# Kernel tuning notes

Measured on AMD Instinct MI355X. Metric: run time of the kernel, lower is better.

The kernel has to match this reference:

```python
import jax, jax.numpy as jnp
import numpy as np

N = 100000
IN_C = 128
HID = 128
LAT = 64
E = 800000


def gcn_conv(x, src, dst, norm, W, b, num_nodes):
    # x: [N, Cin]; src/dst: [E+N] (self-loops appended); norm: [E+N]
    xw = x @ W                                   # [N, Cout]
    msg = xw[src] * norm[:, None]                # gather + scale, [E+N, Cout]
    out = jax.ops.segment_sum(msg, dst, num_segments=num_nodes)
    return out + b


def setup_inputs() -> dict:
    key = jax.random.key(0)
    ks = jax.random.split(key, 8)
    x = jax.random.normal(ks[0], (N, IN_C), dtype=jnp.float32)
    edge_index = jax.random.randint(ks[1], (2, E), 0, N, dtype=jnp.int64)
    batch = jnp.zeros((N,), dtype=jnp.int64)
    # GCNConv params (Glorot-ish scale)
    W1 = jax.random.normal(ks[2], (IN_C, HID), dtype=jnp.float32) / np.sqrt(IN_C)
    b1 = jnp.zeros((HID,), dtype=jnp.float32)
    Wmu = jax.random.normal(ks[3], (HID, LAT), dtype=jnp.float32) / np.sqrt(HID)
    bmu = jnp.zeros((LAT,), dtype=jnp.float32)
    Wlv = jax.random.normal(ks[4], (HID, LAT), dtype=jnp.float32) / np.sqrt(HID)
    blv = jnp.zeros((LAT,), dtype=jnp.float32)
    return {"x": x, "edge_index": edge_index, "batch": batch,
            "W1": W1, "b1": b1, "Wmu": Wmu, "bmu": bmu, "Wlv": Wlv, "blv": blv}


def reference(x, edge_index, batch, W1, b1, Wmu, bmu, Wlv, blv):
    num_nodes = x.shape[0]
    loop = jnp.arange(num_nodes, dtype=edge_index.dtype)
    src = jnp.concatenate([edge_index[0], loop])   # source nodes (+self loops)
    dst = jnp.concatenate([edge_index[1], loop])   # target nodes (+self loops)
    # symmetric GCN normalization: deg over targets, norm = d[src]^-1/2 * d[dst]^-1/2
    deg = jax.ops.segment_sum(jnp.ones_like(dst, dtype=x.dtype), dst,
                              num_segments=num_nodes)
    dis = jnp.where(deg > 0, jax.lax.rsqrt(deg), 0.0)
    norm = dis[src] * dis[dst]                      # [E+N]

    h = jax.nn.relu(gcn_conv(x, src, dst, norm, W1, b1, num_nodes))
    mu = gcn_conv(h, src, dst, norm, Wmu, bmu, num_nodes)
    logvar = gcn_conv(h, src, dst, norm, Wlv, blv, num_nodes)
    return (mu, logvar)
```

## Files before the change

kernel.cpp:

```cpp
#include <hip/hip_runtime.h>

typedef short bf16x8 __attribute__((ext_vector_type(8)));
typedef float f32x4 __attribute__((ext_vector_type(4)));

#define ELLK 32
#define OCAP 4096

static __device__ __forceinline__ float4 f4zero() { return make_float4(0.f, 0.f, 0.f, 0.f); }

static __device__ __forceinline__ unsigned short f2bf(float f) {
  unsigned u = __float_as_uint(f);
  u += 0x7FFFu + ((u >> 16) & 1u);
  return (unsigned short)(u >> 16);
}
static __device__ __forceinline__ float2 bf2x2(unsigned u) {
  float2 r;
  r.x = __uint_as_float(u << 16);
  r.y = __uint_as_float(u & 0xFFFF0000u);
  return r;
}

__global__ void k_setup(const float* __restrict__ W1, const float* __restrict__ Wmu,
                        const float* __restrict__ Wlv, unsigned short* __restrict__ Wt1,
                        unsigned short* __restrict__ Wt2, int* __restrict__ cnt,
                        int* __restrict__ ocount, int n, int nbz) {
  int b = blockIdx.x;
  if (b < nbz) {
    int i = b * 256 + threadIdx.x;
    if (i < n) cnt[i] = 0;
    if (b == 0 && threadIdx.x == 0) *ocount = 0;
  } else {
    int id = (b - nbz) * 256 + threadIdx.x;
    if (id < 16384) {
      int nn = id >> 7, k = id & 127;
      Wt1[id] = f2bf(W1[k * 128 + nn]);
    } else {
      int id2 = id - 16384;
      int nn = id2 >> 7, k = id2 & 127;
      float v = (nn < 64) ? Wmu[k * 64 + nn] : Wlv[k * 64 + (nn - 64)];
      Wt2[id2] = f2bf(v);
    }
  }
}

__global__ __launch_bounds__(256) void k_gemm1_fill(
    const float* __restrict__ x, const unsigned short* __restrict__ Wt,
    unsigned short* __restrict__ A, const int* __restrict__ ei,
    int* __restrict__ cnt, int* __restrict__ ell, int2* __restrict__ ovf,
    int* __restrict__ ocount, int n, int E, int gblk) {
  __shared__ unsigned short Wl[128 * 136];
  __shared__ unsigned short Xl[64 * 136];
  if (blockIdx.x >= gblk) {
    int e = (blockIdx.x - gblk) * 256 + threadIdx.x;
    if (e < E) {
      int s = ei[e];
      int d = ei[E + e];
      int pos = atomicAdd(&cnt[d], 1);
      if (pos < ELLK) {
        ell[d * ELLK + pos] = s;
      } else {
        int o = atomicAdd(ocount, 1);
        if (o < OCAP) ovf[o] = make_int2(d, s);
      }
    }
    return;
  }
  const int tid = threadIdx.x;
  const int row0 = blockIdx.x * 64;
  {
    const uint4* Wg = (const uint4*)Wt;
#pragma unroll
    for (int i = 0; i < 8; ++i) {
      int idx = tid + i * 256;
      int r = idx >> 4, c = idx & 15;
      *(uint4*)&Wl[r * 136 + c * 8] = Wg[r * 16 + c];
    }
  }
  {
#pragma unroll
    for (int i = 0; i < 8; ++i) {
      int idx = tid + i * 256;
      int r = idx >> 5, c = idx & 31;
      int gi = row0 + r;
      float4 v = (gi < n) ? ((const float4*)x)[(size_t)gi * 32 + c] : f4zero();
      ushort4 p;
      p.x = f2bf(v.x); p.y = f2bf(v.y); p.z = f2bf(v.z); p.w = f2bf(v.w);
      *(ushort4*)&Xl[r * 136 + c * 4] = p;
    }
  }
  __syncthreads();

  const int wave = tid >> 6, lane = tid & 63;
  const int li = lane & 15, quad = lane >> 4;
  const int m0 = wave * 16;
  f32x4 acc[8];
#pragma unroll
  for (int t = 0; t < 8; ++t) acc[t] = (f32x4){0.f, 0.f, 0.f, 0.f};

#pragma unroll
  for (int kk = 0; kk < 4; ++kk) {
    int ko = kk * 32 + quad * 8;
    bf16x8 a = *(const bf16x8*)&Xl[(m0 + li) * 136 + ko];
#pragma unroll
    for (int nt = 0; nt < 8; ++nt) {
      bf16x8 b = *(const bf16x8*)&Wl[(nt * 16 + li) * 136 + ko];
      acc[nt] = __builtin_amdgcn_mfma_f32_16x16x32_bf16(a, b, acc[nt], 0, 0, 0);
    }
  }
  __syncthreads();
#pragma unroll
  for (int nt = 0; nt < 8; ++nt)
#pragma unroll
    for (int r = 0; r < 4; ++r)
      Xl[(m0 + quad * 4 + r) * 136 + nt * 16 + li] = f2bf(acc[nt][r]);
  __syncthreads();
  {
    uint4* A4 = (uint4*)A;
#pragma unroll
    for (int i = 0; i < 4; ++i) {
      int idx = tid + i * 256;
      int r = idx >> 4, c = idx & 15;
      int gi = row0 + r;
      if (gi < n) A4[(size_t)gi * 16 + c] = *(uint4*)&Xl[r * 136 + c * 8];
    }
  }
}

template <bool EPI_RELU>
__global__ __launch_bounds__(256) void k_spmm(
    const int* __restrict__ cnt, const int* __restrict__ ell,
    const int2* __restrict__ ovf, const int* __restrict__ ocount,
    const unsigned* __restrict__ S, unsigned* __restrict__ D,
    const float2* __restrict__ bias, int n) {
  int wid = (blockIdx.x * blockDim.x + threadIdx.x) >> 6;
  if (wid >= n) return;
  int lane = threadIdx.x & 63;

  int c = cnt[wid];
  float fc = (float)(c + 1);
  float dsd = rsqrtf(fc);
  float idg = dsd * dsd;
  float2 v = bf2x2(S[(size_t)wid * 64 + lane]);
  float2 acc = make_float2(v.x * idg, v.y * idg);

  const int* row = ell + (size_t)wid * ELLK;
  int m = (c < ELLK) ? c : ELLK;
  int j = 0;
  for (; j + 3 < m; j += 4) {
    int4 ss = *(const int4*)(row + j);
    float n0 = dsd * rsqrtf((float)(cnt[ss.x] + 1));
    float n1 = dsd * rsqrtf((float)(cnt[ss.y] + 1));
    float n2 = dsd * rsqrtf((float)(cnt[ss.z] + 1));
    float n3 = dsd * rsqrtf((float)(cnt[ss.w] + 1));
    float2 u0 = bf2x2(S[(size_t)ss.x * 64 + lane]);
    float2 u1 = bf2x2(S[(size_t)ss.y * 64 + lane]);
    float2 u2 = bf2x2(S[(size_t)ss.z * 64 + lane]);
    float2 u3 = bf2x2(S[(size_t)ss.w * 64 + lane]);
    acc.x = fmaf(n0, u0.x, acc.x); acc.y = fmaf(n0, u0.y, acc.y);
    acc.x = fmaf(n1, u1.x, acc.x); acc.y = fmaf(n1, u1.y, acc.y);
    acc.x = fmaf(n2, u2.x, acc.x); acc.y = fmaf(n2, u2.y, acc.y);
    acc.x = fmaf(n3, u3.x, acc.x); acc.y = fmaf(n3, u3.y, acc.y);
  }
  for (; j < m; ++j) {
    int s = row[j];
    float n0 = dsd * rsqrtf((float)(cnt[s] + 1));
    float2 u0 = bf2x2(S[(size_t)s * 64 + lane]);
    acc.x = fmaf(n0, u0.x, acc.x); acc.y = fmaf(n0, u0.y, acc.y);
  }
  if (c > ELLK) {
    int oc = *ocount;
    if (oc > OCAP) oc = OCAP;
    for (int k = 0; k < oc; ++k) {
      int2 e = ovf[k];
      if (e.x == wid) {
        float n0 = dsd * rsqrtf((float)(cnt[e.y] + 1));
        float2 u0 = bf2x2(S[(size_t)e.y * 64 + lane]);
        acc.x = fmaf(n0, u0.x, acc.x); acc.y = fmaf(n0, u0.y, acc.y);
      }
    }
  }
  if (EPI_RELU) {
    float2 b = bias[lane];
    acc.x = fmaxf(acc.x + b.x, 0.f);
    acc.y = fmaxf(acc.y + b.y, 0.f);
  }
  unsigned pk = (unsigned)f2bf(acc.x) | ((unsigned)f2bf(acc.y) << 16);
  D[(size_t)wid * 64 + lane] = pk;
}

__global__ __launch_bounds__(256) void k_gemm2_mfma(
    const unsigned short* __restrict__ G, const unsigned short* __restrict__ Wt,
    const float* __restrict__ bmu, const float* __restrict__ blv,
    float* __restrict__ out, int n) {
  __shared__ unsigned short Wl[128 * 136];
  __shared__ unsigned short Xl[64 * 136];
  const int tid = threadIdx.x;
  const int row0 = blockIdx.x * 64;
  {
    const uint4* Wg = (const uint4*)Wt;
#pragma unroll
    for (int i = 0; i < 8; ++i) {
      int idx = tid + i * 256;
      int r = idx >> 4, c = idx & 15;
      *(uint4*)&Wl[r * 136 + c * 8] = Wg[r * 16 + c];
    }
  }
  {
    const uint4* Gg = (const uint4*)G;
#pragma unroll
    for (int i = 0; i < 4; ++i) {
      int idx = tid + i * 256;
      int r = idx >> 4, c = idx & 15;
      int gi = row0 + r;
      uint4 v = (gi < n) ? Gg[(size_t)gi * 16 + c] : make_uint4(0, 0, 0, 0);
      *(uint4*)&Xl[r * 136 + c * 8] = v;
    }
  }
  __syncthreads();

  const int wave = tid >> 6, lane = tid & 63;
  const int li = lane & 15, quad = lane >> 4;
  const int m0 = wave * 16;

  float bias[8];
#pragma unroll
  for (int nt = 0; nt < 8; ++nt) {
    int c = nt * 16 + li;
    bias[nt] = (c < 64) ? bmu[c] : blv[c - 64];
  }

  f32x4 acc[8];
#pragma unroll
  for (int t = 0; t < 8; ++t) acc[t] = (f32x4){0.f, 0.f, 0.f, 0.f};

#pragma unroll
  for (int kk = 0; kk < 4; ++kk) {
    int ko = kk * 32 + quad * 8;
    bf16x8 a = *(const bf16x8*)&Xl[(m0 + li) * 136 + ko];
#pragma unroll
    for (int nt = 0; nt < 8; ++nt) {
      bf16x8 b = *(const bf16x8*)&Wl[(nt * 16 + li) * 136 + ko];
      acc[nt] = __builtin_amdgcn_mfma_f32_16x16x32_bf16(a, b, acc[nt], 0, 0, 0);
    }
  }
#pragma unroll
  for (int nt = 0; nt < 8; ++nt) {
    int col = nt * 16 + li;
#pragma unroll
    for (int r = 0; r < 4; ++r) {
      int gi = row0 + m0 + quad * 4 + r;
      if (gi < n) {
        float v = acc[nt][r] + bias[nt];
        if (col < 64) out[(size_t)gi * 64 + col] = v;
        else          out[(size_t)(n + gi) * 64 + (col - 64)] = v;
      }
    }
  }
}

extern "C" void kernel_launch(void* const* d_in, const int* in_sizes, int n_in,
                              void* d_out, int out_size, void* d_ws, size_t ws_size,
                              hipStream_t stream) {
  const float* x   = (const float*)d_in[0];
  const int*   ei  = (const int*)d_in[1];
  const float* W1  = (const float*)d_in[3];
  const float* b1  = (const float*)d_in[4];
  const float* Wmu = (const float*)d_in[5];
  const float* bmu = (const float*)d_in[6];
  const float* Wlv = (const float*)d_in[7];
  const float* blv = (const float*)d_in[8];
  float* out = (float*)d_out;

  const int n = in_sizes[0] / 128;
  const int E = in_sizes[1] / 2;

  float* ws = (float*)d_ws;
  size_t p = 0;
  int* cnt    = (int*)(ws + p); p += n;
  int* ocount = (int*)(ws + p); p += 1;
  p = (p + 3) & ~(size_t)3;
  int* ell    = (int*)(ws + p); p += (size_t)n * ELLK;
  int2* ovf   = (int2*)(ws + p); p += (size_t)OCAP * 2;
  unsigned* A = (unsigned*)(ws + p); p += (size_t)n * 64;
  unsigned* H = (unsigned*)(ws + p); p += (size_t)n * 64;
  unsigned* G = (unsigned*)(ws + p); p += (size_t)n * 64;
  unsigned short* Wt1 = (unsigned short*)(ws + p); p += 8192;
  unsigned short* Wt2 = (unsigned short*)(ws + p); p += 8192;

  int nbz = (n + 255) / 256;
  int eb  = (E + 255) / 256;
  int gblk = (n + 63) / 64;

  k_setup<<<nbz + 128, 256, 0, stream>>>(W1, Wmu, Wlv, Wt1, Wt2, cnt, ocount, n, nbz);
  k_gemm1_fill<<<gblk + eb, 256, 0, stream>>>(x, Wt1, (unsigned short*)A, ei,
                                              cnt, ell, ovf, ocount, n, E, gblk);
  int sblk = (n + 3) / 4;
  k_spmm<true><<<sblk, 256, 0, stream>>>(cnt, ell, ovf, ocount, A, H,
                                         (const float2*)b1, n);
  k_spmm<false><<<sblk, 256, 0, stream>>>(cnt, ell, ovf, ocount, H, G, nullptr, n);
  k_gemm2_mfma<<<gblk, 256, 0, stream>>>((const unsigned short*)G, Wt2, bmu, blv, out, n);
}
```

Measured before the change: 312.3 us.

## Prescale rows by inverse-sqrt degree and pad atomic counters to separate cache lines

Degrees are now computed once into a dnorm array and a packed count/overflow flag array, produced by a new small kernel. The source-side normalization is folded into the GEMM1 epilogue and the SpMM outputs, so the SpMM inner loop becomes plain sums with no per-neighbor count gather or rsqrt. Degree counters are padded to a stride of 16 ints to reduce atomic contention between neighbouring nodes. The cost is that the edge fill no longer overlaps GEMM1, two extra launches are added, and the zeroing pass writes 16x more counter memory.

```diff
diff --git a/kernel.cpp b/kernel.cpp
--- a/kernel.cpp
+++ b/kernel.cpp
@@ -5,6 +5,7 @@
 
 #define ELLK 32
 #define OCAP 4096
+#define CSTRIDE 16
 
 static __device__ __forceinline__ float4 f4zero() { return make_float4(0.f, 0.f, 0.f, 0.f); }
 
@@ -22,12 +23,12 @@
 
 __global__ void k_setup(const float* __restrict__ W1, const float* __restrict__ Wmu,
                         const float* __restrict__ Wlv, unsigned short* __restrict__ Wt1,
-                        unsigned short* __restrict__ Wt2, int* __restrict__ cnt,
-                        int* __restrict__ ocount, int n, int nbz) {
+                        unsigned short* __restrict__ Wt2, uint4* __restrict__ cntz,
+                        int* __restrict__ ocount, int nz4, int nbz) {
   int b = blockIdx.x;
   if (b < nbz) {
     int i = b * 256 + threadIdx.x;
-    if (i < n) cnt[i] = 0;
+    if (i < nz4) cntz[i] = make_uint4(0u, 0u, 0u, 0u);
     if (b == 0 && threadIdx.x == 0) *ocount = 0;
   } else {
     int id = (b - nbz) * 256 + threadIdx.x;
@@ -43,28 +44,37 @@
   }
 }
 
-__global__ __launch_bounds__(256) void k_gemm1_fill(
+__global__ void k_fill(const int* __restrict__ ei, int* __restrict__ cnt,
+                       int* __restrict__ ell, int2* __restrict__ ovf,
+                       int* __restrict__ ocount, int E) {
+  int e = blockIdx.x * 256 + threadIdx.x;
+  if (e >= E) return;
+  int s = ei[e];
+  int d = ei[E + e];
+  int pos = atomicAdd(&cnt[(size_t)d * CSTRIDE], 1);
+  if (pos < ELLK) {
+    ell[(size_t)d * ELLK + pos] = s;
+  } else {
+    int o = atomicAdd(ocount, 1);
+    if (o < OCAP) ovf[o] = make_int2(d, s);
+  }
+}
+
+__global__ void k_dnorm(const int* __restrict__ cnt, float* __restrict__ dnorm,
+                        unsigned* __restrict__ mflag, int n) {
+  int i = blockIdx.x * 256 + threadIdx.x;
+  if (i >= n) return;
+  int c = cnt[(size_t)i * CSTRIDE];
+  dnorm[i] = rsqrtf((float)(c + 1));
+  int m = (c < ELLK) ? c : ELLK;
+  mflag[i] = (unsigned)m | ((c > ELLK) ? 0x80000000u : 0u);
+}
+
+__global__ __launch_bounds__(256) void k_gemm1(
     const float* __restrict__ x, const unsigned short* __restrict__ Wt,
-    unsigned short* __restrict__ A, const int* __restrict__ ei,
-    int* __restrict__ cnt, int* __restrict__ ell, int2* __restrict__ ovf,
-    int* __restrict__ ocount, int n, int E, int gblk) {
+    const float* __restrict__ dnorm, unsigned short* __restrict__ A, int n) {
   __shared__ unsigned short Wl[128 * 136];
   __shared__ unsigned short Xl[64 * 136];
-  if (blockIdx.x >= gblk) {
-    int e = (blockIdx.x - gblk) * 256 + threadIdx.x;
-    if (e < E) {
-      int s = ei[e];
-      int d = ei[E + e];
-      int pos = atomicAdd(&cnt[d], 1);
-      if (pos < ELLK) {
-        ell[d * ELLK + pos] = s;
-      } else {
-        int o = atomicAdd(ocount, 1);
-        if (o < OCAP) ovf[o] = make_int2(d, s);
-      }
-    }
-    return;
-  }
   const int tid = threadIdx.x;
   const int row0 = blockIdx.x * 64;
   {
@@ -107,12 +117,18 @@
       acc[nt] = __builtin_amdgcn_mfma_f32_16x16x32_bf16(a, b, acc[nt], 0, 0, 0);
     }
   }
+  float dn[4];
+#pragma unroll
+  for (int r = 0; r < 4; ++r) {
+    int gi = row0 + m0 + quad * 4 + r;
+    dn[r] = (gi < n) ? dnorm[gi] : 0.f;
+  }
   __syncthreads();
 #pragma unroll
   for (int nt = 0; nt < 8; ++nt)
 #pragma unroll
     for (int r = 0; r < 4; ++r)
-      Xl[(m0 + quad * 4 + r) * 136 + nt * 16 + li] = f2bf(acc[nt][r]);
+      Xl[(m0 + quad * 4 + r) * 136 + nt * 16 + li] = f2bf(acc[nt][r] * dn[r]);
   __syncthreads();
   {
     uint4* A4 = (uint4*)A;
@@ -128,63 +144,58 @@
 
 template <bool EPI_RELU>
 __global__ __launch_bounds__(256) void k_spmm(
-    const int* __restrict__ cnt, const int* __restrict__ ell,
-    const int2* __restrict__ ovf, const int* __restrict__ ocount,
-    const unsigned* __restrict__ S, unsigned* __restrict__ D,
-    const float2* __restrict__ bias, int n) {
+    const unsigned* __restrict__ mflag, const float* __restrict__ dnorm,
+    const int* __restrict__ ell, const int2* __restrict__ ovf,
+    const int* __restrict__ ocount, const unsigned* __restrict__ S,
+    unsigned* __restrict__ D, const float2* __restrict__ bias, int n) {
   int wid = (blockIdx.x * blockDim.x + threadIdx.x) >> 6;
   if (wid >= n) return;
   int lane = threadIdx.x & 63;
 
-  int c = cnt[wid];
-  float fc = (float)(c + 1);
-  float dsd = rsqrtf(fc);
-  float idg = dsd * dsd;
-  float2 v = bf2x2(S[(size_t)wid * 64 + lane]);
-  float2 acc = make_float2(v.x * idg, v.y * idg);
+  unsigned mf = mflag[wid];
+  int m = (int)(mf & 0xFFFFu);
+  float dsd = dnorm[wid];
+  float2 acc = bf2x2(S[(size_t)wid * 64 + lane]);
 
   const int* row = ell + (size_t)wid * ELLK;
-  int m = (c < ELLK) ? c : ELLK;
   int j = 0;
   for (; j + 3 < m; j += 4) {
     int4 ss = *(const int4*)(row + j);
-    float n0 = dsd * rsqrtf((float)(cnt[ss.x] + 1));
-    float n1 = dsd * rsqrtf((float)(cnt[ss.y] + 1));
-    float n2 = dsd * rsqrtf((float)(cnt[ss.z] + 1));
-    float n3 = dsd * rsqrtf((float)(cnt[ss.w] + 1));
     float2 u0 = bf2x2(S[(size_t)ss.x * 64 + lane]);
     float2 u1 = bf2x2(S[(size_t)ss.y * 64 + lane]);
     float2 u2 = bf2x2(S[(size_t)ss.z * 64 + lane]);
     float2 u3 = bf2x2(S[(size_t)ss.w * 64 + lane]);
-    acc.x = fmaf(n0, u0.x, acc.x); acc.y = fmaf(n0, u0.y, acc.y);
-    acc.x = fmaf(n1, u1.x, acc.x); acc.y = fmaf(n1, u1.y, acc.y);
-    acc.x = fmaf(n2, u2.x, acc.x); acc.y = fmaf(n2, u2.y, acc.y);
-    acc.x = fmaf(n3, u3.x, acc.x); acc.y = fmaf(n3, u3.y, acc.y);
+    acc.x += u0.x + u1.x + u2.x + u3.x;
+    acc.y += u0.y + u1.y + u2.y + u3.y;
   }
   for (; j < m; ++j) {
     int s = row[j];
-    float n0 = dsd * rsqrtf((float)(cnt[s] + 1));
     float2 u0 = bf2x2(S[(size_t)s * 64 + lane]);
-    acc.x = fmaf(n0, u0.x, acc.x); acc.y = fmaf(n0, u0.y, acc.y);
-  }
-  if (c > ELLK) {
+    acc.x += u0.x;
+    acc.y += u0.y;
+  }
+  if (mf & 0x80000000u) {
     int oc = *ocount;
     if (oc > OCAP) oc = OCAP;
     for (int k = 0; k < oc; ++k) {
       int2 e = ovf[k];
       if (e.x == wid) {
-        float n0 = dsd * rsqrtf((float)(cnt[e.y] + 1));
         float2 u0 = bf2x2(S[(size_t)e.y * 64 + lane]);
-        acc.x = fmaf(n0, u0.x, acc.x); acc.y = fmaf(n0, u0.y, acc.y);
+        acc.x += u0.x;
+        acc.y += u0.y;
       }
     }
   }
+  float2 o;
   if (EPI_RELU) {
     float2 b = bias[lane];
-    acc.x = fmaxf(acc.x + b.x, 0.f);
-    acc.y = fmaxf(acc.y + b.y, 0.f);
-  }
-  unsigned pk = (unsigned)f2bf(acc.x) | ((unsigned)f2bf(acc.y) << 16);
+    o.x = dsd * fmaxf(fmaf(dsd, acc.x, b.x), 0.f);
+    o.y = dsd * fmaxf(fmaf(dsd, acc.y, b.y), 0.f);
+  } else {
+    o.x = dsd * acc.x;
+    o.y = dsd * acc.y;
+  }
+  unsigned pk = (unsigned)f2bf(o.x) | ((unsigned)f2bf(o.y) << 16);
   D[(size_t)wid * 64 + lane] = pk;
 }
 
@@ -276,7 +287,7 @@
 
   float* ws = (float*)d_ws;
   size_t p = 0;
-  int* cnt    = (int*)(ws + p); p += n;
+  int* cnt    = (int*)(ws + p); p += (size_t)n * CSTRIDE;
   int* ocount = (int*)(ws + p); p += 1;
   p = (p + 3) & ~(size_t)3;
   int* ell    = (int*)(ws + p); p += (size_t)n * ELLK;
@@ -286,17 +297,22 @@
   unsigned* G = (unsigned*)(ws + p); p += (size_t)n * 64;
   unsigned short* Wt1 = (unsigned short*)(ws + p); p += 8192;
   unsigned short* Wt2 = (unsigned short*)(ws + p); p += 8192;
-
-  int nbz = (n + 255) / 256;
-  int eb  = (E + 255) / 256;
+  float* dnorm    = (float*)(ws + p); p += n;
+  unsigned* mflag = (unsigned*)(ws + p); p += n;
+
+  int nz4  = (n * CSTRIDE) / 4;
+  int nbz  = (nz4 + 255) / 256;
+  int eb   = (E + 255) / 256;
   int gblk = (n + 63) / 64;
-
-  k_setup<<<nbz + 128, 256, 0, stream>>>(W1, Wmu, Wlv, Wt1, Wt2, cnt, ocount, n, nbz);
-  k_gemm1_fill<<<gblk + eb, 256, 0, stream>>>(x, Wt1, (unsigned short*)A, ei,
-                                              cnt, ell, ovf, ocount, n, E, gblk);
+  int nb   = (n + 255) / 256;
   int sblk = (n + 3) / 4;
-  k_spmm<true><<<sblk, 256, 0, stream>>>(cnt, ell, ovf, ocount, A, H,
+
+  k_setup<<<nbz + 128, 256, 0, stream>>>(W1, Wmu, Wlv, Wt1, Wt2, (uint4*)cnt, ocount, nz4, nbz);
+  k_fill<<<eb, 256, 0, stream>>>(ei, cnt, ell, ovf, ocount, E);
+  k_dnorm<<<nb, 256, 0, stream>>>(cnt, dnorm, mflag, n);
+  k_gemm1<<<gblk, 256, 0, stream>>>(x, Wt1, dnorm, (unsigned short*)A, n);
+  k_spmm<true><<<sblk, 256, 0, stream>>>(mflag, dnorm, ell, ovf, ocount, A, H,
                                          (const float2*)b1, n);
-  k_spmm<false><<<sblk, 256, 0, stream>>>(cnt, ell, ovf, ocount, H, G, nullptr, n);
+  k_spmm<false><<<sblk, 256, 0, stream>>>(mflag, dnorm, ell, ovf, ocount, H, G, nullptr, n);
   k_gemm2_mfma<<<gblk, 256, 0, stream>>>((const unsigned short*)G, Wt2, bmu, blv, out, n);
 }
```

After: 300.2 us. 1.04x faster.
